# Optimization experiments

Hardware: AMD Instinct MI355X
Metric: run time of the kernel (lower is better)

Reference implementation:

```python
import jax, jax.numpy as jnp
from jax import lax
import numpy as np

B, T, H, E = 64, 256, 1024, 1024  # batch, seq_len, input/hidden size, embedded_dim


def setup_inputs() -> dict:
    key = jax.random.key(0)
    ks = jax.random.split(key, 9)
    s_ih = 1.0 / np.sqrt(H)
    inp = {
        "x": jax.random.normal(ks[0], (B, T, H), dtype=jnp.float32),
        # GRU params (PyTorch layout: gates stacked [r; z; n])
        "w_ih": jax.random.uniform(ks[1], (3 * H, H), minval=-s_ih, maxval=s_ih, dtype=jnp.float32),
        "w_hh": jax.random.uniform(ks[2], (3 * H, H), minval=-s_ih, maxval=s_ih, dtype=jnp.float32),
        "b_ih": jax.random.uniform(ks[3], (3 * H,), minval=-s_ih, maxval=s_ih, dtype=jnp.float32),
        "b_hh": jax.random.uniform(ks[4], (3 * H,), minval=-s_ih, maxval=s_ih, dtype=jnp.float32),
        # fc1: H -> H, fc2: H -> E
        "w1": jax.random.uniform(ks[5], (H, H), minval=-s_ih, maxval=s_ih, dtype=jnp.float32),
        "b1": jax.random.uniform(ks[6], (H,), minval=-s_ih, maxval=s_ih, dtype=jnp.float32),
        "w2": jax.random.uniform(ks[7], (E, H), minval=-s_ih, maxval=s_ih, dtype=jnp.float32),
        "b2": jax.random.uniform(ks[8], (E,), minval=-s_ih, maxval=s_ih, dtype=jnp.float32),
    }
    return inp


def _gru_last_hidden(x, w_ih, w_hh, b_ih, b_hh):
    # Precompute all input-side gate projections in one big GEMM: [B,T,3H]
    x_gates = jnp.einsum("bth,gh->btg", x, w_ih) + b_ih
    h0 = jnp.zeros((x.shape[0], w_hh.shape[1]), x.dtype)

    def step(h, xg):
        hg = h @ w_hh.T + b_hh  # [B, 3H]
        xr, xz, xn = jnp.split(xg, 3, axis=-1)
        hr, hz, hn = jnp.split(hg, 3, axis=-1)
        r = jax.nn.sigmoid(xr + hr)
        z = jax.nn.sigmoid(xz + hz)
        n = jnp.tanh(xn + r * hn)
        h_new = (1.0 - z) * n + z * h
        return h_new, None

    h_final, _ = lax.scan(step, h0, jnp.swapaxes(x_gates, 0, 1))  # scan over time
    return h_final  # [B, H]


def reference(x, w_ih, w_hh, b_ih, b_hh, w1, b1, w2, b2):
    h = _gru_last_hidden(x, w_ih, w_hh, b_ih, b_hh)
    h = jax.nn.leaky_relu(h @ w1.T + b1, negative_slope=0.2)
    return h @ w2.T + b2  # [B, E]
```

## Files before the change

kernel.cpp:

```cpp
#include <hip/hip_runtime.h>
#include <cstdint>
#include <cstddef>

constexpr int B_ = 64;
constexpr int T_ = 256;
constexpr int H_ = 1024;
constexpr int E_ = 1024;
constexpr int G3 = 3 * H_;

typedef __attribute__((ext_vector_type(8))) short short8;
typedef __attribute__((ext_vector_type(4))) float f32x4;

__device__ __forceinline__ f32x4 mfma16(short8 a, short8 b, f32x4 c) {
  return __builtin_amdgcn_mfma_f32_16x16x32_bf16(a, b, c, 0, 0, 0);
}

__device__ __forceinline__ void bf16_split(float f, unsigned short& hi, unsigned short& lo) {
  unsigned u = __float_as_uint(f);
  unsigned r = u + 0x7fff + ((u >> 16) & 1);
  hi = (unsigned short)(r >> 16);
  float fhi = __uint_as_float((unsigned)hi << 16);
  float res = f - fhi;
  unsigned v = __float_as_uint(res);
  unsigned s = v + 0x7fff + ((v >> 16) & 1);
  lo = (unsigned short)(s >> 16);
}

__global__ __launch_bounds__(256, 2) void xgates_gemm(
    const float* __restrict__ A,
    const float* __restrict__ Bw,
    const float* __restrict__ bias,
    float* __restrict__ C)
{
  constexpr int BM = 128, BN = 128, BK = 32, K = 1024;
  __shared__ float As[BK][BM + 4];
  __shared__ float Bs[BK][BN + 4];
  const int bm = blockIdx.x * BM;
  const int bn = blockIdx.y * BN;
  const int tid = threadIdx.x;
  const int tx = tid & 15;
  const int ty = tid >> 4;

  float acc[8][8];
#pragma unroll
  for (int i = 0; i < 8; i++)
#pragma unroll
    for (int j = 0; j < 8; j++) acc[i][j] = 0.f;

  float4 pa[4], pb[4];
  auto gload = [&](int k0) {
#pragma unroll
    for (int i = 0; i < 4; i++) {
      int idx = tid + i * 256;
      int r   = idx >> 3;
      int c4  = (idx & 7) * 4;
      pa[i] = *reinterpret_cast<const float4*>(&A[(size_t)(bm + r) * K + k0 + c4]);
      pb[i] = *reinterpret_cast<const float4*>(&Bw[(size_t)(bn + r) * K + k0 + c4]);
    }
  };

  gload(0);
  for (int k0 = 0; k0 < K; k0 += BK) {
    if (k0) __syncthreads();
#pragma unroll
    for (int i = 0; i < 4; i++) {
      int idx = tid + i * 256;
      int r   = idx >> 3;
      int c4  = (idx & 7) * 4;
      As[c4 + 0][r] = pa[i].x; As[c4 + 1][r] = pa[i].y;
      As[c4 + 2][r] = pa[i].z; As[c4 + 3][r] = pa[i].w;
      Bs[c4 + 0][r] = pb[i].x; Bs[c4 + 1][r] = pb[i].y;
      Bs[c4 + 2][r] = pb[i].z; Bs[c4 + 3][r] = pb[i].w;
    }
    __syncthreads();
    if (k0 + BK < K) gload(k0 + BK);
#pragma unroll 8
    for (int kk = 0; kk < BK; kk++) {
      float a[8], b[8];
      *reinterpret_cast<float4*>(&a[0]) = *reinterpret_cast<const float4*>(&As[kk][tx * 8]);
      *reinterpret_cast<float4*>(&a[4]) = *reinterpret_cast<const float4*>(&As[kk][tx * 8 + 4]);
      *reinterpret_cast<float4*>(&b[0]) = *reinterpret_cast<const float4*>(&Bs[kk][ty * 8]);
      *reinterpret_cast<float4*>(&b[4]) = *reinterpret_cast<const float4*>(&Bs[kk][ty * 8 + 4]);
#pragma unroll
      for (int i = 0; i < 8; i++)
#pragma unroll
        for (int j = 0; j < 8; j++)
          acc[i][j] = fmaf(a[i], b[j], acc[i][j]);
    }
  }

#pragma unroll
  for (int i = 0; i < 8; i++) {
    int m = bm + tx * 8 + i;
    int b = m >> 8;
    int t = m & 255;
    float* crow = &C[((size_t)t * 64 + b) * G3 + bn + ty * 8];
#pragma unroll
    for (int j4 = 0; j4 < 2; j4++) {
      float4 v;
      v.x = acc[i][j4 * 4 + 0] + bias[bn + ty * 8 + j4 * 4 + 0];
      v.y = acc[i][j4 * 4 + 1] + bias[bn + ty * 8 + j4 * 4 + 1];
      v.z = acc[i][j4 * 4 + 2] + bias[bn + ty * 8 + j4 * 4 + 2];
      v.w = acc[i][j4 * 4 + 3] + bias[bn + ty * 8 + j4 * 4 + 3];
      *reinterpret_cast<float4*>(&crow[j4 * 4]) = v;
    }
  }
}

__global__ __launch_bounds__(256) void prep_wfrag(
    const float* __restrict__ w_hh,
    unsigned short* __restrict__ whi,
    unsigned short* __restrict__ wlo)
{
  int d = blockIdx.x * 256 + threadIdx.x;
  int l    = d & 63;
  int slot = d >> 6;
  int kf   = slot & 31;
  int bg   = slot >> 5;
  int g    = bg % 3;
  int blk  = bg / 3;
  int row  = g * 1024 + blk * 16 + (l & 15);
  int k0   = kf * 32 + (l >> 4) * 8;
  const float* src = w_hh + (size_t)row * 1024 + k0;
  short8 vh, vl;
#pragma unroll
  for (int j = 0; j < 8; j++) {
    unsigned short h, lo;
    bf16_split(src[j], h, lo);
    vh[j] = (short)h;
    vl[j] = (short)lo;
  }
  *reinterpret_cast<short8*>(whi + (size_t)d * 8) = vh;
  *reinterpret_cast<short8*>(wlo + (size_t)d * 8) = vl;
}

__global__ __launch_bounds__(256) void gru_step_mfma(
    const float* __restrict__ xg_t,
    const float* __restrict__ ht_in,
    float* __restrict__ ht_out,
    const unsigned short* __restrict__ whi,
    const unsigned short* __restrict__ wlo,
    const unsigned short* __restrict__ hhi_in,
    const unsigned short* __restrict__ hlo_in,
    unsigned short* __restrict__ hhi_out,
    unsigned short* __restrict__ hlo_out,
    const float* __restrict__ b_hh)
{
  __shared__ f32x4 args[3][4][4][64];
  const int tid  = threadIdx.x;
  const int lane = tid & 63;
  const int wid  = __builtin_amdgcn_readfirstlane(tid >> 6);
  const int blk  = blockIdx.x;
  const int u0   = blk * 16;

  const int bcol  = wid * 16 + (lane & 15);
  const int urow0 = (lane >> 4) * 4;
  float xr[4], xz[4], xn[4], hprev[4], bhr[4], bhz[4], bhn[4];
#pragma unroll
  for (int r = 0; r < 4; r++) {
    int u = u0 + urow0 + r;
    xr[r]    = xg_t[(size_t)bcol * G3 + u];
    xz[r]    = xg_t[(size_t)bcol * G3 + 1024 + u];
    xn[r]    = xg_t[(size_t)bcol * G3 + 2048 + u];
    hprev[r] = ht_in[(size_t)u * 64 + bcol];
    bhr[r]   = b_hh[u];
    bhz[r]   = b_hh[1024 + u];
    bhn[r]   = b_hh[2048 + u];
  }

  f32x4 acc[3][4];
#pragma unroll
  for (int g = 0; g < 3; g++)
#pragma unroll
    for (int nt = 0; nt < 4; nt++) acc[g][nt] = (f32x4){0.f, 0.f, 0.f, 0.f};

  for (int kk = 0; kk < 8; kk++) {
    const int kf = wid * 8 + kk;
    short8 Ah[3], Al[3], Bh[4], Bl[4];
#pragma unroll
    for (int g = 0; g < 3; g++) {
      size_t off = ((size_t)((blk * 3 + g) * 32 + kf) * 64 + lane) * 8;
      Ah[g] = *reinterpret_cast<const short8*>(whi + off);
      Al[g] = *reinterpret_cast<const short8*>(wlo + off);
    }
#pragma unroll
    for (int nt = 0; nt < 4; nt++) {
      size_t off = ((size_t)(kf * 4 + nt) * 64 + lane) * 8;
      Bh[nt] = *reinterpret_cast<const short8*>(hhi_in + off);
      Bl[nt] = *reinterpret_cast<const short8*>(hlo_in + off);
    }
#pragma unroll
    for (int g = 0; g < 3; g++)
#pragma unroll
      for (int nt = 0; nt < 4; nt++) {
        acc[g][nt] = mfma16(Ah[g], Bh[nt], acc[g][nt]);
        acc[g][nt] = mfma16(Ah[g], Bl[nt], acc[g][nt]);
        acc[g][nt] = mfma16(Al[g], Bh[nt], acc[g][nt]);
        acc[g][nt] = mfma16(Al[g], Bl[nt], acc[g][nt]);
      }
  }

#pragma unroll
  for (int g = 0; g < 3; g++)
#pragma unroll
    for (int nt = 0; nt < 4; nt++) args[g][nt][wid][lane] = acc[g][nt];
  __syncthreads();

  f32x4 cg[3];
#pragma unroll
  for (int g = 0; g < 3; g++) {
    f32x4 s = args[g][wid][0][lane];
    s += args[g][wid][1][lane];
    s += args[g][wid][2][lane];
    s += args[g][wid][3][lane];
    cg[g] = s;
  }

#pragma unroll
  for (int r = 0; r < 4; r++) {
    float hr = cg[0][r] + bhr[r];
    float hz = cg[1][r] + bhz[r];
    float hn = cg[2][r] + bhn[r];
    float rr = 1.f / (1.f + expf(-(xr[r] + hr)));
    float zz = 1.f / (1.f + expf(-(xz[r] + hz)));
    float nn = tanhf(xn[r] + rr * hn);
    float h  = (1.f - zz) * nn + zz * hprev[r];

    const int u = u0 + urow0 + r;
    ht_out[(size_t)u * 64 + bcol] = h;

    unsigned short hi, lo;
    bf16_split(h, hi, lo);
    const int kf  = u >> 5;
    const int kin = u & 31;
    const int lp  = ((kin >> 3) << 4) | (bcol & 15);
    const int nt  = bcol >> 4;
    size_t off = ((size_t)(kf * 4 + nt) * 64 + lp) * 8 + (kin & 7);
    hhi_out[off] = hi;
    hlo_out[off] = lo;
  }
}

template <int LEAKY, int STORE_T>
__global__ __launch_bounds__(256) void fc_kernel(
    const float* __restrict__ At,
    const float* __restrict__ W,
    const float* __restrict__ bias,
    float* __restrict__ out,
    int N, int K)
{
  constexpr int KC = 128;
  __shared__ float a_s[KC][68];
  const int tid  = threadIdx.x;
  const int lane = tid & 63;
  const int wid  = __builtin_amdgcn_readfirstlane(tid >> 6);
  const int n0   = blockIdx.x * 16 + wid * 4;

  const float* __restrict__ w0 = W + (size_t)(n0 + 0) * K;
  const float* __restrict__ w1 = W + (size_t)(n0 + 1) * K;
  const float* __restrict__ w2 = W + (size_t)(n0 + 2) * K;
  const float* __restrict__ w3 = W + (size_t)(n0 + 3) * K;

  float acc0 = 0.f, acc1 = 0.f, acc2 = 0.f, acc3 = 0.f;
  for (int kc = 0; kc < K; kc += KC) {
#pragma unroll
    for (int i = 0; i < 8; i++) {
      int idx = tid + i * 256;
      int j   = idx >> 4;
      int c4  = (idx & 15) * 4;
      *reinterpret_cast<float4*>(&a_s[j][c4]) =
          *reinterpret_cast<const float4*>(&At[(size_t)(kc + j) * 64 + c4]);
    }
    __syncthreads();
#pragma unroll 16
    for (int j = 0; j < KC; j++) {
      float av = a_s[j][lane];
      acc0 = fmaf(av, w0[kc + j], acc0);
      acc1 = fmaf(av, w1[kc + j], acc1);
      acc2 = fmaf(av, w2[kc + j], acc2);
      acc3 = fmaf(av, w3[kc + j], acc3);
    }
    __syncthreads();
  }
  float r0 = acc0 + bias[n0 + 0];
  float r1 = acc1 + bias[n0 + 1];
  float r2 = acc2 + bias[n0 + 2];
  float r3 = acc3 + bias[n0 + 3];
  if (LEAKY) {
    r0 = (r0 >= 0.f) ? r0 : 0.2f * r0;
    r1 = (r1 >= 0.f) ? r1 : 0.2f * r1;
    r2 = (r2 >= 0.f) ? r2 : 0.2f * r2;
    r3 = (r3 >= 0.f) ? r3 : 0.2f * r3;
  }
  if (STORE_T) {
    out[(size_t)(n0 + 0) * 64 + lane] = r0;
    out[(size_t)(n0 + 1) * 64 + lane] = r1;
    out[(size_t)(n0 + 2) * 64 + lane] = r2;
    out[(size_t)(n0 + 3) * 64 + lane] = r3;
  } else {
    float4 v; v.x = r0; v.y = r1; v.z = r2; v.w = r3;
    *reinterpret_cast<float4*>(&out[(size_t)lane * N + n0]) = v;
  }
}

extern "C" void kernel_launch(void* const* d_in, const int* in_sizes, int n_in,
                              void* d_out, int out_size, void* d_ws, size_t ws_size,
                              hipStream_t stream) {
  (void)in_sizes; (void)n_in; (void)out_size; (void)ws_size;
  const float* x    = (const float*)d_in[0];
  const float* w_ih = (const float*)d_in[1];
  const float* w_hh = (const float*)d_in[2];
  const float* b_ih = (const float*)d_in[3];
  const float* b_hh = (const float*)d_in[4];
  const float* w1   = (const float*)d_in[5];
  const float* b1   = (const float*)d_in[6];
  const float* w2   = (const float*)d_in[7];
  const float* b2   = (const float*)d_in[8];
  float* out = (float*)d_out;

  float* ws = (float*)d_ws;
  float* xg = ws;
  float* hA = xg + (size_t)T_ * B_ * G3;
  float* hB = hA + (size_t)H_ * B_;
  float* y1 = hB + (size_t)H_ * B_;
  unsigned short* whi = (unsigned short*)(y1 + (size_t)H_ * B_);
  unsigned short* wlo = whi + (size_t)G3 * H_;
  unsigned short* hf  = wlo + (size_t)G3 * H_;
  unsigned short* hhi0 = hf;
  unsigned short* hlo0 = hhi0 + 65536;
  unsigned short* hhi1 = hlo0 + 65536;
  unsigned short* hlo1 = hhi1 + 65536;

  hipMemsetAsync(hA, 0, (size_t)H_ * B_ * sizeof(float), stream);
  hipMemsetAsync(hhi0, 0, 2 * 65536 * sizeof(unsigned short), stream);

  prep_wfrag<<<1536, 256, 0, stream>>>(w_hh, whi, wlo);
  xgates_gemm<<<dim3(128, 24), 256, 0, stream>>>(x, w_ih, b_ih, xg);

  for (int t = 0; t < T_; t++) {
    const float* hin  = (t & 1) ? hB : hA;
    float*       hout = (t & 1) ? hA : hB;
    const unsigned short* fhi_in  = (t & 1) ? hhi1 : hhi0;
    const unsigned short* flo_in  = (t & 1) ? hlo1 : hlo0;
    unsigned short*       fhi_out = (t & 1) ? hhi0 : hhi1;
    unsigned short*       flo_out = (t & 1) ? hlo0 : hlo1;
    gru_step_mfma<<<64, 256, 0, stream>>>(xg + (size_t)t * B_ * G3, hin, hout,
                                          whi, wlo, fhi_in, flo_in, fhi_out, flo_out,
                                          b_hh);
  }
  fc_kernel<1, 1><<<64, 256, 0, stream>>>(hA, w1, b1, y1, H_, H_);
  fc_kernel<0, 0><<<64, 256, 0, stream>>>(y1, w2, b2, out, E_, H_);
}
```

Before: 4.059 ms.

## Fuse GRU time loop into persistent kernel with grid-wide atomic barrier

Replaces the 256 per-timestep kernel launches with a single persistent kernel of 64 blocks. The blocks synchronise between steps through an atomic counter barrier, and the hidden state stays in registers. Hidden-state fragments are exchanged through relaxed agent-scope atomic 8-byte loads and stores, with double-buffered prefetch of the next k-slice. This removes launch overhead and the fp32 hidden round-trip, but relies on all 64 blocks being co-resident and adds spin-wait latency each step.

```diff
diff --git a/kernel.cpp b/kernel.cpp
--- a/kernel.cpp
+++ b/kernel.cpp
@@ -1,6 +1,7 @@
 #include <hip/hip_runtime.h>
 #include <cstdint>
 #include <cstddef>
+#include <cstring>
 
 constexpr int B_ = 64;
 constexpr int T_ = 256;
@@ -24,6 +25,13 @@
   unsigned v = __float_as_uint(res);
   unsigned s = v + 0x7fff + ((v >> 16) & 1);
   lo = (unsigned short)(s >> 16);
+}
+
+__device__ __forceinline__ void frag_store8(unsigned short* p, unsigned long long v) {
+  __hip_atomic_store((unsigned long long*)(void*)p, v, __ATOMIC_RELAXED, __HIP_MEMORY_SCOPE_AGENT);
+}
+__device__ __forceinline__ unsigned long long frag_load8(const unsigned short* p) {
+  return __hip_atomic_load((const unsigned long long*)(const void*)p, __ATOMIC_RELAXED, __HIP_MEMORY_SCOPE_AGENT);
 }
 
 __global__ __launch_bounds__(256, 2) void xgates_gemm(
@@ -134,17 +142,15 @@
   *reinterpret_cast<short8*>(wlo + (size_t)d * 8) = vl;
 }
 
-__global__ __launch_bounds__(256) void gru_step_mfma(
-    const float* __restrict__ xg_t,
-    const float* __restrict__ ht_in,
-    float* __restrict__ ht_out,
+__global__ __launch_bounds__(256) void gru_scan(
+    const float* __restrict__ xg,
+    float* __restrict__ h_final,
     const unsigned short* __restrict__ whi,
     const unsigned short* __restrict__ wlo,
-    const unsigned short* __restrict__ hhi_in,
-    const unsigned short* __restrict__ hlo_in,
-    unsigned short* __restrict__ hhi_out,
-    unsigned short* __restrict__ hlo_out,
-    const float* __restrict__ b_hh)
+    unsigned short* __restrict__ f0h, unsigned short* __restrict__ f0l,
+    unsigned short* __restrict__ f1h, unsigned short* __restrict__ f1l,
+    const float* __restrict__ b_hh,
+    unsigned* __restrict__ cnt)
 {
   __shared__ f32x4 args[3][4][4][64];
   const int tid  = threadIdx.x;
@@ -155,89 +161,150 @@
 
   const int bcol  = wid * 16 + (lane & 15);
   const int urow0 = (lane >> 4) * 4;
-  float xr[4], xz[4], xn[4], hprev[4], bhr[4], bhz[4], bhn[4];
+
+  float bhr[4], bhz[4], bhn[4];
 #pragma unroll
   for (int r = 0; r < 4; r++) {
     int u = u0 + urow0 + r;
-    xr[r]    = xg_t[(size_t)bcol * G3 + u];
-    xz[r]    = xg_t[(size_t)bcol * G3 + 1024 + u];
-    xn[r]    = xg_t[(size_t)bcol * G3 + 2048 + u];
-    hprev[r] = ht_in[(size_t)u * 64 + bcol];
-    bhr[r]   = b_hh[u];
-    bhz[r]   = b_hh[1024 + u];
-    bhn[r]   = b_hh[2048 + u];
-  }
-
-  f32x4 acc[3][4];
-#pragma unroll
-  for (int g = 0; g < 3; g++)
-#pragma unroll
-    for (int nt = 0; nt < 4; nt++) acc[g][nt] = (f32x4){0.f, 0.f, 0.f, 0.f};
-
-  for (int kk = 0; kk < 8; kk++) {
-    const int kf = wid * 8 + kk;
-    short8 Ah[3], Al[3], Bh[4], Bl[4];
+    bhr[r] = b_hh[u];
+    bhz[r] = b_hh[1024 + u];
+    bhn[r] = b_hh[2048 + u];
+  }
+  const int u_s  = u0 + urow0;
+  const int kf_s = u_s >> 5;
+  const int j0_s = u_s & 7;
+  const int lp_s = (((u_s & 31) >> 3) << 4) | (bcol & 15);
+  const int nt_s = bcol >> 4;
+  const size_t off_s = ((size_t)(kf_s * 4 + nt_s) * 64 + lp_s) * 8 + j0_s;
+
+  float h_prev[4] = {0.f, 0.f, 0.f, 0.f};
+
+  for (int t = 0; t < T_; t++) {
+    const unsigned short* hhi_in = (t & 1) ? f1h : f0h;
+    const unsigned short* hlo_in = (t & 1) ? f1l : f0l;
+    unsigned short* hhi_out = (t & 1) ? f0h : f1h;
+    unsigned short* hlo_out = (t & 1) ? f0l : f1l;
+    const float* xg_t = xg + (size_t)t * B_ * G3;
+
+    float xr[4], xz[4], xn[4];
+#pragma unroll
+    for (int r = 0; r < 4; r++) {
+      int u = u0 + urow0 + r;
+      xr[r] = xg_t[(size_t)bcol * G3 + u];
+      xz[r] = xg_t[(size_t)bcol * G3 + 1024 + u];
+      xn[r] = xg_t[(size_t)bcol * G3 + 2048 + u];
+    }
+
+    f32x4 acc[3][4];
+#pragma unroll
+    for (int g = 0; g < 3; g++)
+#pragma unroll
+      for (int nt = 0; nt < 4; nt++) acc[g][nt] = (f32x4){0.f, 0.f, 0.f, 0.f};
+
+    unsigned long long bq[2][16];
+    {
+      const int kf = wid * 8;
+#pragma unroll
+      for (int nt = 0; nt < 4; nt++) {
+        const unsigned short* bh = hhi_in + ((size_t)(kf * 4 + nt) * 64 + lane) * 8;
+        const unsigned short* bl = hlo_in + ((size_t)(kf * 4 + nt) * 64 + lane) * 8;
+        bq[0][nt * 4 + 0] = frag_load8(bh);
+        bq[0][nt * 4 + 1] = frag_load8(bh + 4);
+        bq[0][nt * 4 + 2] = frag_load8(bl);
+        bq[0][nt * 4 + 3] = frag_load8(bl + 4);
+      }
+    }
+#pragma unroll
+    for (int kk = 0; kk < 8; kk++) {
+      const int kf = wid * 8 + kk;
+      if (kk < 7) {
+        const int kf2 = kf + 1;
+#pragma unroll
+        for (int nt = 0; nt < 4; nt++) {
+          const unsigned short* bh = hhi_in + ((size_t)(kf2 * 4 + nt) * 64 + lane) * 8;
+          const unsigned short* bl = hlo_in + ((size_t)(kf2 * 4 + nt) * 64 + lane) * 8;
+          bq[(kk + 1) & 1][nt * 4 + 0] = frag_load8(bh);
+          bq[(kk + 1) & 1][nt * 4 + 1] = frag_load8(bh + 4);
+          bq[(kk + 1) & 1][nt * 4 + 2] = frag_load8(bl);
+          bq[(kk + 1) & 1][nt * 4 + 3] = frag_load8(bl + 4);
+        }
+      }
+      short8 Ah[3], Al[3];
+#pragma unroll
+      for (int g = 0; g < 3; g++) {
+        size_t off = ((size_t)((blk * 3 + g) * 32 + kf) * 64 + lane) * 8;
+        Ah[g] = *reinterpret_cast<const short8*>(whi + off);
+        Al[g] = *reinterpret_cast<const short8*>(wlo + off);
+      }
+#pragma unroll
+      for (int nt = 0; nt < 4; nt++) {
+        union { unsigned long long q[2]; short8 v; } Bh, Bl;
+        Bh.q[0] = bq[kk & 1][nt * 4 + 0]; Bh.q[1] = bq[kk & 1][nt * 4 + 1];
+        Bl.q[0] = bq[kk & 1][nt * 4 + 2]; Bl.q[1] = bq[kk & 1][nt * 4 + 3];
+#pragma unroll
+        for (int g = 0; g < 3; g++) {
+          acc[g][nt] = mfma16(Ah[g], Bh.v, acc[g][nt]);
+          acc[g][nt] = mfma16(Ah[g], Bl.v, acc[g][nt]);
+          acc[g][nt] = mfma16(Al[g], Bh.v, acc[g][nt]);
+          acc[g][nt] = mfma16(Al[g], Bl.v, acc[g][nt]);
+        }
+      }
+    }
+
+#pragma unroll
+    for (int g = 0; g < 3; g++)
+#pragma unroll
+      for (int nt = 0; nt < 4; nt++) args[g][nt][wid][lane] = acc[g][nt];
+    __syncthreads();
+
+    f32x4 cg[3];
 #pragma unroll
     for (int g = 0; g < 3; g++) {
-      size_t off = ((size_t)((blk * 3 + g) * 32 + kf) * 64 + lane) * 8;
-      Ah[g] = *reinterpret_cast<const short8*>(whi + off);
-      Al[g] = *reinterpret_cast<const short8*>(wlo + off);
-    }
-#pragma unroll
-    for (int nt = 0; nt < 4; nt++) {
-      size_t off = ((size_t)(kf * 4 + nt) * 64 + lane) * 8;
-      Bh[nt] = *reinterpret_cast<const short8*>(hhi_in + off);
-      Bl[nt] = *reinterpret_cast<const short8*>(hlo_in + off);
-    }
-#pragma unroll
-    for (int g = 0; g < 3; g++)
-#pragma unroll
-      for (int nt = 0; nt < 4; nt++) {
-        acc[g][nt] = mfma16(Ah[g], Bh[nt], acc[g][nt]);
-        acc[g][nt] = mfma16(Ah[g], Bl[nt], acc[g][nt]);
-        acc[g][nt] = mfma16(Al[g], Bh[nt], acc[g][nt]);
-        acc[g][nt] = mfma16(Al[g], Bl[nt], acc[g][nt]);
+      f32x4 s = args[g][wid][0][lane];
+      s += args[g][wid][1][lane];
+      s += args[g][wid][2][lane];
+      s += args[g][wid][3][lane];
+      cg[g] = s;
+    }
+
+    unsigned short hi4[4], lo4[4];
+#pragma unroll
+    for (int r = 0; r < 4; r++) {
+      float hr = cg[0][r] + bhr[r];
+      float hz = cg[1][r] + bhz[r];
+      float hn = cg[2][r] + bhn[r];
+      float rr = 1.f / (1.f + expf(-(xr[r] + hr)));
+      float zz = 1.f / (1.f + expf(-(xz[r] + hz)));
+      float nn = tanhf(xn[r] + rr * hn);
+      float h  = (1.f - zz) * nn + zz * h_prev[r];
+      h_prev[r] = h;
+      bf16_split(h, hi4[r], lo4[r]);
+    }
+    unsigned long long hv = (unsigned long long)hi4[0] | ((unsigned long long)hi4[1] << 16) |
+                            ((unsigned long long)hi4[2] << 32) | ((unsigned long long)hi4[3] << 48);
+    unsigned long long lv = (unsigned long long)lo4[0] | ((unsigned long long)lo4[1] << 16) |
+                            ((unsigned long long)lo4[2] << 32) | ((unsigned long long)lo4[3] << 48);
+    frag_store8(hhi_out + off_s, hv);
+    frag_store8(hlo_out + off_s, lv);
+
+    if (t == T_ - 1) {
+#pragma unroll
+      for (int r = 0; r < 4; r++)
+        h_final[(size_t)(u0 + urow0 + r) * 64 + bcol] = h_prev[r];
+    }
+
+    if (t < T_ - 1) {
+      __syncthreads();
+      if (tid == 0) {
+        __hip_atomic_fetch_add(cnt, 1u, __ATOMIC_RELEASE, __HIP_MEMORY_SCOPE_AGENT);
+        const unsigned target = (unsigned)(t + 1) * 64u;
+        while (__hip_atomic_load(cnt, __ATOMIC_RELAXED, __HIP_MEMORY_SCOPE_AGENT) < target) {
+          __builtin_amdgcn_s_sleep(1);
+        }
+        __builtin_amdgcn_fence(__ATOMIC_ACQUIRE, "agent");
       }
-  }
-
-#pragma unroll
-  for (int g = 0; g < 3; g++)
-#pragma unroll
-    for (int nt = 0; nt < 4; nt++) args[g][nt][wid][lane] = acc[g][nt];
-  __syncthreads();
-
-  f32x4 cg[3];
-#pragma unroll
-  for (int g = 0; g < 3; g++) {
-    f32x4 s = args[g][wid][0][lane];
-    s += args[g][wid][1][lane];
-    s += args[g][wid][2][lane];
-    s += args[g][wid][3][lane];
-    cg[g] = s;
-  }
-
-#pragma unroll
-  for (int r = 0; r < 4; r++) {
-    float hr = cg[0][r] + bhr[r];
-    float hz = cg[1][r] + bhz[r];
-    float hn = cg[2][r] + bhn[r];
-    float rr = 1.f / (1.f + expf(-(xr[r] + hr)));
-    float zz = 1.f / (1.f + expf(-(xz[r] + hz)));
-    float nn = tanhf(xn[r] + rr * hn);
-    float h  = (1.f - zz) * nn + zz * hprev[r];
-
-    const int u = u0 + urow0 + r;
-    ht_out[(size_t)u * 64 + bcol] = h;
-
-    unsigned short hi, lo;
-    bf16_split(h, hi, lo);
-    const int kf  = u >> 5;
-    const int kin = u & 31;
-    const int lp  = ((kin >> 3) << 4) | (bcol & 15);
-    const int nt  = bcol >> 4;
-    size_t off = ((size_t)(kf * 4 + nt) * 64 + lp) * 8 + (kin & 7);
-    hhi_out[off] = hi;
-    hlo_out[off] = lo;
+      __syncthreads();
+    }
   }
 }
 
@@ -318,36 +385,26 @@
   const float* b2   = (const float*)d_in[8];
   float* out = (float*)d_out;
 
-  float* ws = (float*)d_ws;
-  float* xg = ws;
-  float* hA = xg + (size_t)T_ * B_ * G3;
-  float* hB = hA + (size_t)H_ * B_;
-  float* y1 = hB + (size_t)H_ * B_;
-  unsigned short* whi = (unsigned short*)(y1 + (size_t)H_ * B_);
-  unsigned short* wlo = whi + (size_t)G3 * H_;
-  unsigned short* hf  = wlo + (size_t)G3 * H_;
-  unsigned short* hhi0 = hf;
-  unsigned short* hlo0 = hhi0 + 65536;
-  unsigned short* hhi1 = hlo0 + 65536;
-  unsigned short* hlo1 = hhi1 + 65536;
-
-  hipMemsetAsync(hA, 0, (size_t)H_ * B_ * sizeof(float), stream);
-  hipMemsetAsync(hhi0, 0, 2 * 65536 * sizeof(unsigned short), stream);
+  char* p = (char*)d_ws;
+  float* xg = (float*)p;            p += (size_t)T_ * B_ * G3 * 4;
+  float* hF = (float*)p;            p += (size_t)H_ * B_ * 4;
+  float* y1 = (float*)p;            p += (size_t)H_ * B_ * 4;
+  unsigned short* whi = (unsigned short*)p; p += (size_t)G3 * H_ * 2;
+  unsigned short* wlo = (unsigned short*)p; p += (size_t)G3 * H_ * 2;
+  unsigned short* f0h = (unsigned short*)p; p += 65536 * 2;
+  unsigned short* f0l = (unsigned short*)p; p += 65536 * 2;
+  unsigned short* f1h = (unsigned short*)p; p += 65536 * 2;
+  unsigned short* f1l = (unsigned short*)p; p += 65536 * 2;
+  unsigned* cnt = (unsigned*)p;     p += 256;
+
+  hipMemsetAsync(f0h, 0, 2 * 65536 * 2, stream);
+  hipMemsetAsync(cnt, 0, 256, stream);
 
   prep_wfrag<<<1536, 256, 0, stream>>>(w_hh, whi, wlo);
   xgates_gemm<<<dim3(128, 24), 256, 0, stream>>>(x, w_ih, b_ih, xg);
 
-  for (int t = 0; t < T_; t++) {
-    const float* hin  = (t & 1) ? hB : hA;
-    float*       hout = (t & 1) ? hA : hB;
-    const unsigned short* fhi_in  = (t & 1) ? hhi1 : hhi0;
-    const unsigned short* flo_in  = (t & 1) ? hlo1 : hlo0;
-    unsigned short*       fhi_out = (t & 1) ? hhi0 : hhi1;
-    unsigned short*       flo_out = (t & 1) ? hlo0 : hlo1;
-    gru_step_mfma<<<64, 256, 0, stream>>>(xg + (size_t)t * B_ * G3, hin, hout,
-                                          whi, wlo, fhi_in, flo_in, fhi_out, flo_out,
-                                          b_hh);
-  }
-  fc_kernel<1, 1><<<64, 256, 0, stream>>>(hA, w1, b1, y1, H_, H_);
+  gru_scan<<<64, 256, 0, stream>>>(xg, hF, whi, wlo, f0h, f0l, f1h, f1l, b_hh, cnt);
+
+  fc_kernel<1, 1><<<64, 256, 0, stream>>>(hF, w1, b1, y1, H_, H_);
   fc_kernel<0, 0><<<64, 256, 0, stream>>>(y1, w2, b2, out, E_, H_);
 }
```

New measurement: 5.014 ms. 23.5% more time.
